# Optimization experiments

Measured on AMD Instinct MI355X. Metric: run time of the kernel, lower is better.

## Reference

```python
import jax, jax.numpy as jnp
import numpy as np

BN_EPS = 1e-5


def conv2d(x, w, b, stride, pad):
    # x: [N,C,H,W], w: [O,I,kh,kw]
    y = jax.lax.conv_general_dilated(
        x, w, window_strides=(stride, stride),
        padding=[(pad, pad), (pad, pad)],
        dimension_numbers=('NCHW', 'OIHW', 'NCHW'))
    return y + b[None, :, None, None]


def batchnorm(x, gamma, beta):
    # training-mode BN: batch stats over (N,H,W) per channel
    m = x.mean(axis=(0, 2, 3), keepdims=True)
    v = x.var(axis=(0, 2, 3), keepdims=True)
    xn = (x - m) * jax.lax.rsqrt(v + BN_EPS)
    return gamma[None, :, None, None] * xn + beta[None, :, None, None]


def setup_inputs() -> dict:
    key = jax.random.key(0)
    ks = jax.random.split(key, 8)
    H = W = 1024
    x = jax.random.normal(ks[0], (1, 3, H, W), dtype=jnp.float32)
    # conv1: 3 -> 32, k3
    w1 = jax.random.normal(ks[1], (32, 3, 3, 3), dtype=jnp.float32) * 0.1
    b1 = jnp.zeros((32,), jnp.float32)
    # conv2: 1 -> 16, k3 s2 p2
    w2 = jax.random.normal(ks[2], (16, 1, 3, 3), dtype=jnp.float32) * 0.1
    b2 = jnp.zeros((16,), jnp.float32)
    g2 = jnp.ones((16,), jnp.float32)
    bt2 = jnp.zeros((16,), jnp.float32)
    # conv3: 16 -> 32, k3 s2 p2
    w3 = jax.random.normal(ks[3], (32, 16, 3, 3), dtype=jnp.float32) * 0.1
    b3 = jnp.zeros((32,), jnp.float32)
    g3 = jnp.ones((32,), jnp.float32)
    bt3 = jnp.zeros((32,), jnp.float32)
    return {'x': x, 'w1': w1, 'b1': b1, 'w2': w2, 'b2': b2, 'g2': g2,
            'bt2': bt2, 'w3': w3, 'b3': b3, 'g3': g3, 'bt3': bt3}


def reference(x, w1, b1, w2, b2, g2, bt2, w3, b3, g3, bt3):
    out = conv2d(x, w1, b1, stride=1, pad=2)          # [1,32,H+2,W+2]
    f = out[0]                                         # [32,H',W'] (Gram uses batch 0 only)
    gram = jnp.einsum('chw,dhw->cd', f, f)             # [32,32] single GEMM instead of O(n^2) loop
    gram = gram[None, None, :, :]                      # [1,1,32,32]
    h = jax.nn.relu(batchnorm(conv2d(gram, w2, b2, stride=2, pad=2), g2, bt2))  # [1,16,17,17]
    h = jax.nn.relu(batchnorm(conv2d(h, w3, b3, stride=2, pad=2), g3, bt3))     # [1,32,10,10]
    return h.mean(axis=(2, 3), keepdims=True)          # AdaptiveAvgPool2d((1,1)) -> [1,32,1,1]
```

## Files before the change

kernel.cpp:

```cpp
#include <hip/hip_runtime.h>

#define NTILES_X 65
#define NTILES   (65*65)
#define OHW      1026
#define NCHUNK   32
#define NBLK     1024
#define NXCD     8
#define BAND     529

typedef unsigned int  uint;
typedef unsigned short ushort;
typedef float  floatx16 __attribute__((ext_vector_type(16)));
typedef __bf16 bf16x8   __attribute__((ext_vector_type(8)));

__device__ __forceinline__ uint pk2f(float a, float b) {
    ushort lo = __builtin_bit_cast(ushort, (__bf16)a);
    ushort hi = __builtin_bit_cast(ushort, (__bf16)b);
    return (uint)lo | ((uint)hi << 16);
}
__device__ __forceinline__ bf16x8 frag_of(uint a, uint b, uint c, uint d) {
    uint4 u = make_uint4(a, b, c, d);
    return __builtin_bit_cast(bf16x8, u);
}
__device__ __forceinline__ constexpr int koff_of(int k) {
    return (k / 9) * 324 + ((k % 9) / 3) * 18 + (k % 3);
}
__device__ __forceinline__ uint bslot(const ushort* buf, int base, int h, int ka, int kb) {
    if (kb < 27) {
        int off = h ? koff_of(kb) : koff_of(ka);
        return (uint)buf[base + off];
    } else if (ka < 27) {
        uint cst = (kb == 27) ? 0x3F80u : 0u;
        uint rd  = (uint)buf[base + koff_of(ka)];
        return h ? cst : rd;
    } else {
        uint ca  = (ka == 27) ? 0x3F80u : 0u;
        uint cb2 = (kb == 27) ? 0x3F80u : 0u;
        return h ? cb2 : ca;
    }
}

__global__ __launch_bounds__(256, 4) void k_conv_gram(
    const float* __restrict__ x,
    const float* __restrict__ w1,
    const float* __restrict__ b1,
    float* __restrict__ partial,
    int nblk)
{
    __shared__ __align__(16) ushort sInB[2][976];
    __shared__ __align__(16) float  gep[4096];

    const int t    = threadIdx.x;
    const int wv   = t >> 6;
    const int lane = t & 63;
    const int h    = lane >> 5;
    const int c    = lane & 31;

    const float b1c = b1[c];
    uint wu0[4], wu1[4];
#pragma unroll
    for (int q = 0; q < 4; ++q) {
        {
            int k0 = h * 8 + 2 * q;
            wu0[q] = pk2f(w1[c * 27 + k0], w1[c * 27 + k0 + 1]);
        }
        {
            int k0 = 16 + h * 8 + 2 * q, k1 = k0 + 1;
            float r0 = w1[c * 27 + (k0 < 27 ? k0 : 26)];
            float r1 = w1[c * 27 + (k1 < 27 ? k1 : 26)];
            float v0 = (k0 < 27) ? r0 : (k0 == 27 ? b1c : 0.f);
            float v1 = (k1 < 27) ? r1 : (k1 == 27 ? b1c : 0.f);
            wu1[q] = pk2f(v0, v1);
        }
    }

    floatx16 gacc;
#pragma unroll
    for (int i = 0; i < 16; ++i) gacc[i] = 0.f;

    const int xcd    = blockIdx.x & (NXCD - 1);
    const int lb     = blockIdx.x >> 3;
    const int nb_per = nblk >> 3;
    const int tstart = xcd * BAND;
    const int tend   = (tstart + BAND < NTILES) ? tstart + BAND : NTILES;

    auto loadregs = [&](int tile, float* v) {
        const int ty = tile / NTILES_X;
        const int tx = tile - ty * NTILES_X;
        const int by = ty * 16, bx = tx * 16;
        const bool interior = (ty >= 1) & (ty <= 62) & (tx >= 1) & (tx <= 62);
#pragma unroll
        for (int j = 0; j < 4; ++j) {
            const int i = t + 256 * j;
            if (j == 3 && i >= 972) { v[j] = 0.f; continue; }
            int ic = i / 324, rem = i - ic * 324, r = rem / 18, cc = rem - r * 18;
            if (interior) {
                v[j] = x[ic * 1048576 + (by - 2 + r) * 1024 + (bx - 2 + cc)];
            } else {
                int iy = by - 2 + r, ix = bx - 2 + cc;
                v[j] = ((unsigned)iy < 1024u && (unsigned)ix < 1024u)
                         ? x[ic * 1048576 + iy * 1024 + ix] : 0.f;
            }
        }
    };
    auto writebuf = [&](int buf, const float* v) {
#pragma unroll
        for (int j = 0; j < 4; ++j) {
            const int i = t + 256 * j;
            if (j == 3 && i >= 972) continue;
            sInB[buf][i] = __builtin_bit_cast(ushort, (__bf16)v[j]);
        }
    };

    int tile = tstart + lb;
    int cur  = 0;
    {
        float v[4];
        loadregs(tile, v);
        writebuf(0, v);
    }
    __syncthreads();

    for (; tile < tend; ) {
        const int nxt = tile + nb_per;
        const bool hasNext = nxt < tend;
        float vn[4];
        if (hasNext) loadregs(nxt, vn);

        {
            const int ty = tile / NTILES_X;
            const int tx = tile - ty * NTILES_X;
            const int by = ty * 16, bx = tx * 16;
            const bool needmask = (ty == 64) | (tx == 64);
            const ushort* bufp = &sInB[cur][0];

#pragma unroll
            for (int e = 0; e < 2; ++e) {
                const int cb   = 2 * wv + e;
                const int base = (cb * 2 + (c >> 4)) * 18 + (c & 15);

                floatx16 cacc;
#pragma unroll
                for (int i = 0; i < 16; ++i) cacc[i] = 0.f;

                uint bu[4];
#pragma unroll
                for (int q = 0; q < 4; ++q) {
                    uint lo = bslot(bufp, base, h, 2*q,     2*q + 8);
                    uint hi = bslot(bufp, base, h, 2*q + 1, 2*q + 9);
                    bu[q] = lo | (hi << 16);
                }
                cacc = __builtin_amdgcn_mfma_f32_32x32x16_bf16(
                    frag_of(bu[0], bu[1], bu[2], bu[3]),
                    frag_of(wu0[0], wu0[1], wu0[2], wu0[3]), cacc, 0, 0, 0);
#pragma unroll
                for (int q = 0; q < 4; ++q) {
                    uint lo = bslot(bufp, base, h, 16 + 2*q,     16 + 2*q + 8);
                    uint hi = bslot(bufp, base, h, 16 + 2*q + 1, 16 + 2*q + 9);
                    bu[q] = lo | (hi << 16);
                }
                cacc = __builtin_amdgcn_mfma_f32_32x32x16_bf16(
                    frag_of(bu[0], bu[1], bu[2], bu[3]),
                    frag_of(wu1[0], wu1[1], wu1[2], wu1[3]), cacc, 0, 0, 0);

                uint pa[4], pb[4];
#pragma unroll
                for (int q2 = 0; q2 < 4; ++q2) {
                    pa[q2] = pk2f(cacc[2*q2],     cacc[2*q2 + 1]);
                    pb[q2] = pk2f(cacc[8 + 2*q2], cacc[8 + 2*q2 + 1]);
                }
                if (needmask) {
                    const uint rA = (uint)((by + 2*cb)     < OHW);
                    const uint rB = (uint)((by + 2*cb + 1) < OHW);
#pragma unroll
                    for (int q2 = 0; q2 < 4; ++q2) {
                        const int q  = q2 >> 1, mm = 2 * (q2 & 1);
                        const uint x0 = (uint)((bx + 8*q + 4*h + mm)     < OHW);
                        const uint x1 = (uint)((bx + 8*q + 4*h + mm + 1) < OHW);
                        pa[q2] &= ((rA & x0) ? 0x0000FFFFu : 0u) | ((rA & x1) ? 0xFFFF0000u : 0u);
                        pb[q2] &= ((rB & x0) ? 0x0000FFFFu : 0u) | ((rB & x1) ? 0xFFFF0000u : 0u);
                    }
                }
                bf16x8 fa = frag_of(pa[0], pa[1], pa[2], pa[3]);
                bf16x8 fb = frag_of(pb[0], pb[1], pb[2], pb[3]);
                gacc = __builtin_amdgcn_mfma_f32_32x32x16_bf16(fa, fa, gacc, 0, 0, 0);
                gacc = __builtin_amdgcn_mfma_f32_32x32x16_bf16(fb, fb, gacc, 0, 0, 0);
            }
        }

        if (hasNext) writebuf(cur ^ 1, vn);
        __syncthreads();
        cur ^= 1;
        tile = nxt;
    }

#pragma unroll
    for (int r = 0; r < 16; ++r) {
        const int row = (r & 3) + 8 * (r >> 2) + 4 * h;
        gep[wv * 1024 + row * 32 + c] = gacc[r];
    }
    __syncthreads();
    {
        const int e = t * 4;
        float s[4] = {0.f, 0.f, 0.f, 0.f};
#pragma unroll
        for (int w = 0; w < 4; ++w) {
            float v[4];
            *(float4*)v = *(const float4*)&gep[w * 1024 + e];
#pragma unroll
            for (int j = 0; j < 4; ++j) s[j] += v[j];
        }
        *(float4*)&partial[(size_t)blockIdx.x * 1024 + e] = *(float4*)s;
    }
}

__global__ __launch_bounds__(256) void k_reduce(
    const float* __restrict__ partial, float* __restrict__ partial2, int nblk)
{
    const int gt    = blockIdx.x * 256 + threadIdx.x;
    const int e     = gt & 1023;
    const int chunk = gt >> 10;
    float s = 0.f;
    for (int b = chunk; b < nblk; b += NCHUNK) s += partial[(size_t)b * 1024 + e];
    partial2[chunk * 1024 + e] = s;
}

__global__ __launch_bounds__(1024) void k_mid(
    const float* __restrict__ partial2,
    const float* __restrict__ w2, const float* __restrict__ b2,
    const float* __restrict__ g2, const float* __restrict__ bt2,
    float* __restrict__ y1pG)
{
    __shared__ float G_pad[36 * 36];
    __shared__ float y1[16 * 289];
    __shared__ float m1[16], r1[16];
    __shared__ float sw2[144], sp2[48];

    const int t = threadIdx.x;

    float s0 = 0.f, s1 = 0.f, s2 = 0.f, s3 = 0.f;
#pragma unroll
    for (int k = 0; k < NCHUNK; k += 4) {
        s0 += partial2[(k + 0) * 1024 + t];
        s1 += partial2[(k + 1) * 1024 + t];
        s2 += partial2[(k + 2) * 1024 + t];
        s3 += partial2[(k + 3) * 1024 + t];
    }
    const float g = (s0 + s1) + (s2 + s3);

    for (int i = t; i < 1296; i += 1024) G_pad[i] = 0.f;
    for (int i = t; i < 144; i += 1024) sw2[i] = w2[i];
    if (t < 16)              sp2[t] = b2[t];
    else if (t < 32)         sp2[t] = g2[t - 16];
    else if (t < 48)         sp2[t] = bt2[t - 32];
    __syncthreads();

    G_pad[((t >> 5) + 2) * 36 + (t & 31) + 2] = g;
    __syncthreads();

    for (int idx = t; idx < 16 * 289; idx += 1024) {
        const int oc = idx / 289;
        const int r  = idx - oc * 289;
        const int oy = r / 17, ox = r - (r / 17) * 17;
        const float* gp = &G_pad[(2 * oy) * 36 + 2 * ox];
        const float* wr = &sw2[oc * 9];
        float s = sp2[oc];
#pragma unroll
        for (int ky = 0; ky < 3; ++ky)
#pragma unroll
            for (int kx = 0; kx < 3; ++kx)
                s = fmaf(gp[ky * 36 + kx], wr[ky * 3 + kx], s);
        y1[idx] = s;
    }
    __syncthreads();

    {
        const int ch = t >> 6, j = t & 63;
        float s = 0.f, ss = 0.f;
        for (int i = j; i < 289; i += 64) {
            float v = y1[ch * 289 + i];
            s += v; ss += v * v;
        }
#pragma unroll
        for (int o = 32; o; o >>= 1) { s += __shfl_xor(s, o); ss += __shfl_xor(ss, o); }
        if (j == 0) {
            float m = s * (1.f / 289.f);
            float var = ss * (1.f / 289.f) - m * m;
            m1[ch] = m;
            r1[ch] = rsqrtf(var + 1e-5f);
        }
    }
    __syncthreads();

    for (int idx = t; idx < 16 * 441; idx += 1024) {
        const int ic  = idx / 441;
        const int rem = idx - ic * 441;
        const int yy  = rem / 21, xx = rem - yy * 21;
        float v = 0.f;
        if (yy >= 2 && yy < 19 && xx >= 2 && xx < 19) {
            float raw = y1[ic * 289 + (yy - 2) * 17 + (xx - 2)];
            v = (raw - m1[ic]) * r1[ic] * sp2[16 + ic] + sp2[32 + ic];
            v = v > 0.f ? v : 0.f;
        }
        y1pG[idx] = v;
    }
}

__global__ __launch_bounds__(256) void k_c3(
    const float* __restrict__ y1pG,
    const float* __restrict__ w3, const float* __restrict__ b3,
    const float* __restrict__ g3, const float* __restrict__ bt3,
    float* __restrict__ out)
{
    __shared__ float yL[16 * 441];
    __shared__ float y2L[128];

    const int t  = threadIdx.x;
    const int oc = blockIdx.x;

    for (int i = t; i < 7056; i += 256) yL[i] = y1pG[i];
    if (t >= 100 && t < 128) y2L[t] = 0.f;
    __syncthreads();

    if (t < 100) {
        const int oy = t / 10, ox = t - 10 * (t / 10);
        const float* wr = w3 + oc * 144;
        float a0 = b3[oc], a1 = 0.f, a2 = 0.f;
#pragma unroll
        for (int ic = 0; ic < 16; ++ic) {
            const float* yi = &yL[ic * 441 + (2 * oy) * 21 + 2 * ox];
            const float* wi = wr + ic * 9;
#pragma unroll
            for (int kx = 0; kx < 3; ++kx) {
                a0 = fmaf(yi[kx],      wi[kx],     a0);
                a1 = fmaf(yi[21 + kx], wi[3 + kx], a1);
                a2 = fmaf(yi[42 + kx], wi[6 + kx], a2);
            }
        }
        y2L[t] = (a0 + a1) + a2;
    }
    __syncthreads();

    if (t < 64) {
        const float x0 = y2L[t], x1 = y2L[t + 64];
        float s = x0 + x1, ss = x0 * x0 + x1 * x1;
#pragma unroll
        for (int o = 32; o; o >>= 1) { s += __shfl_xor(s, o); ss += __shfl_xor(ss, o); }
        const float m  = s * 0.01f;
        const float var = ss * 0.01f - m * m;
        const float rs = rsqrtf(var + 1e-5f);
        const float gg = g3[oc], bb = bt3[oc];
        float a = 0.f;
        if (t < 100) { float f = (x0 - m) * rs * gg + bb; a += f > 0.f ? f : 0.f; }
        if (t < 36)  { float f = (x1 - m) * rs * gg + bb; a += f > 0.f ? f : 0.f; }
#pragma unroll
        for (int o = 32; o; o >>= 1) a += __shfl_xor(a, o);
        if (t == 0) out[oc] = a * 0.01f;
    }
}

extern "C" void kernel_launch(void* const* d_in, const int* in_sizes, int n_in,
                              void* d_out, int out_size, void* d_ws, size_t ws_size,
                              hipStream_t stream)
{
    const float* x   = (const float*)d_in[0];
    const float* w1  = (const float*)d_in[1];
    const float* b1  = (const float*)d_in[2];
    const float* w2  = (const float*)d_in[3];
    const float* b2  = (const float*)d_in[4];
    const float* g2  = (const float*)d_in[5];
    const float* bt2 = (const float*)d_in[6];
    const float* w3  = (const float*)d_in[7];
    const float* b3  = (const float*)d_in[8];
    const float* g3  = (const float*)d_in[9];
    const float* bt3 = (const float*)d_in[10];

    int nblk = NBLK;

    float* P    = (float*)d_ws;
    float* P2   = P + (size_t)nblk * 1024;
    float* y1pG = P2 + (size_t)NCHUNK * 1024;
    float* out  = (float*)d_out;

    k_conv_gram<<<nblk, 256, 0, stream>>>(x, w1, b1, P, nblk);
    k_reduce<<<128, 256, 0, stream>>>(P, P2, nblk);
    k_mid<<<1, 1024, 0, stream>>>(P2, w2, b2, g2, bt2, y1pG);
    k_c3<<<32, 256, 0, stream>>>(y1pG, w3, b3, g3, bt3, out);
}
```

Before: 41.58 us.

## Fuse mid-stage and conv3 tail into one kernel with redundant per-block compute

Merges the single-block conv2/BN stage and the 32-block conv3/BN/pool kernel into one launch. Each of the 32 blocks now recomputes the Gram reduction, conv2 and BN2 redundantly in shared memory, so the global round-trip of the padded intermediate and one kernel launch go away. Conv3 is also split across two thread groups over input channels and then summed. The cost is 32x redundant small compute and larger shared memory per block.

Result: faster. 39.39 us (-5.3%).

```diff
diff --git a/kernel.cpp b/kernel.cpp
--- a/kernel.cpp
+++ b/kernel.cpp
@@ -225,46 +225,55 @@
     partial2[chunk * 1024 + e] = s;
 }
 
-__global__ __launch_bounds__(1024) void k_mid(
+__global__ __launch_bounds__(256) void k_tail2(
     const float* __restrict__ partial2,
     const float* __restrict__ w2, const float* __restrict__ b2,
     const float* __restrict__ g2, const float* __restrict__ bt2,
-    float* __restrict__ y1pG)
+    const float* __restrict__ w3, const float* __restrict__ b3,
+    const float* __restrict__ g3, const float* __restrict__ bt3,
+    float* __restrict__ out)
 {
     __shared__ float G_pad[36 * 36];
     __shared__ float y1[16 * 289];
+    __shared__ float y1p[16 * 21 * 21];
+    __shared__ float y2L[256];
     __shared__ float m1[16], r1[16];
     __shared__ float sw2[144], sp2[48];
 
-    const int t = threadIdx.x;
-
-    float s0 = 0.f, s1 = 0.f, s2 = 0.f, s3 = 0.f;
-#pragma unroll
-    for (int k = 0; k < NCHUNK; k += 4) {
-        s0 += partial2[(k + 0) * 1024 + t];
-        s1 += partial2[(k + 1) * 1024 + t];
-        s2 += partial2[(k + 2) * 1024 + t];
-        s3 += partial2[(k + 3) * 1024 + t];
-    }
-    const float g = (s0 + s1) + (s2 + s3);
-
-    for (int i = t; i < 1296; i += 1024) G_pad[i] = 0.f;
-    for (int i = t; i < 144; i += 1024) sw2[i] = w2[i];
-    if (t < 16)              sp2[t] = b2[t];
-    else if (t < 32)         sp2[t] = g2[t - 16];
-    else if (t < 48)         sp2[t] = bt2[t - 32];
-    __syncthreads();
-
-    G_pad[((t >> 5) + 2) * 36 + (t & 31) + 2] = g;
-    __syncthreads();
-
-    for (int idx = t; idx < 16 * 289; idx += 1024) {
-        const int oc = idx / 289;
-        const int r  = idx - oc * 289;
+    const int t  = threadIdx.x;
+    const int oc = blockIdx.x;
+
+    float gv[4] = {0.f, 0.f, 0.f, 0.f};
+#pragma unroll
+    for (int k = 0; k < NCHUNK; ++k) {
+        float v[4];
+        *(float4*)v = *(const float4*)&partial2[k * 1024 + t * 4];
+#pragma unroll
+        for (int j = 0; j < 4; ++j) gv[j] += v[j];
+    }
+
+    for (int i = t; i < 1296; i += 256) G_pad[i] = 0.f;
+    for (int i = t; i < 7056; i += 256) y1p[i] = 0.f;
+    if (t < 144) sw2[t] = w2[t];
+    if (t >= 160 && t < 176)      sp2[t - 160]      = b2[t - 160];
+    else if (t >= 176 && t < 192) sp2[t - 160]      = g2[t - 176];
+    else if (t >= 192 && t < 208) sp2[t - 160]      = bt2[t - 192];
+    __syncthreads();
+
+#pragma unroll
+    for (int j = 0; j < 4; ++j) {
+        const int e = t * 4 + j;
+        G_pad[((e >> 5) + 2) * 36 + (e & 31) + 2] = gv[j];
+    }
+    __syncthreads();
+
+    for (int idx = t; idx < 16 * 289; idx += 256) {
+        const int c2 = idx / 289;
+        const int r  = idx - c2 * 289;
         const int oy = r / 17, ox = r - (r / 17) * 17;
         const float* gp = &G_pad[(2 * oy) * 36 + 2 * ox];
-        const float* wr = &sw2[oc * 9];
-        float s = sp2[oc];
+        const float* wr = &sw2[c2 * 9];
+        float s = sp2[c2];
 #pragma unroll
         for (int ky = 0; ky < 3; ++ky)
 #pragma unroll
@@ -275,14 +284,16 @@
     __syncthreads();
 
     {
-        const int ch = t >> 6, j = t & 63;
+        const int lane = t & 63;
+        const int ch   = (t >> 6) * 4 + (lane >> 4);
+        const int j    = lane & 15;
         float s = 0.f, ss = 0.f;
-        for (int i = j; i < 289; i += 64) {
+        for (int i = j; i < 289; i += 16) {
             float v = y1[ch * 289 + i];
             s += v; ss += v * v;
         }
 #pragma unroll
-        for (int o = 32; o; o >>= 1) { s += __shfl_xor(s, o); ss += __shfl_xor(ss, o); }
+        for (int o = 8; o; o >>= 1) { s += __shfl_xor(s, o); ss += __shfl_xor(ss, o); }
         if (j == 0) {
             float m = s * (1.f / 289.f);
             float var = ss * (1.f / 289.f) - m * m;
@@ -292,53 +303,41 @@
     }
     __syncthreads();
 
-    for (int idx = t; idx < 16 * 441; idx += 1024) {
-        const int ic  = idx / 441;
-        const int rem = idx - ic * 441;
-        const int yy  = rem / 21, xx = rem - yy * 21;
-        float v = 0.f;
-        if (yy >= 2 && yy < 19 && xx >= 2 && xx < 19) {
-            float raw = y1[ic * 289 + (yy - 2) * 17 + (xx - 2)];
-            v = (raw - m1[ic]) * r1[ic] * sp2[16 + ic] + sp2[32 + ic];
-            v = v > 0.f ? v : 0.f;
-        }
-        y1pG[idx] = v;
-    }
-}
-
-__global__ __launch_bounds__(256) void k_c3(
-    const float* __restrict__ y1pG,
-    const float* __restrict__ w3, const float* __restrict__ b3,
-    const float* __restrict__ g3, const float* __restrict__ bt3,
-    float* __restrict__ out)
-{
-    __shared__ float yL[16 * 441];
-    __shared__ float y2L[128];
-
-    const int t  = threadIdx.x;
-    const int oc = blockIdx.x;
-
-    for (int i = t; i < 7056; i += 256) yL[i] = y1pG[i];
+    for (int idx = t; idx < 16 * 289; idx += 256) {
+        const int c2 = idx / 289;
+        const int r  = idx - c2 * 289;
+        const int oy = r / 17, ox = r - (r / 17) * 17;
+        float v = (y1[idx] - m1[c2]) * r1[c2] * sp2[16 + c2] + sp2[32 + c2];
+        y1p[c2 * 441 + (oy + 2) * 21 + ox + 2] = v > 0.f ? v : 0.f;
+    }
     if (t >= 100 && t < 128) y2L[t] = 0.f;
     __syncthreads();
 
-    if (t < 100) {
-        const int oy = t / 10, ox = t - 10 * (t / 10);
-        const float* wr = w3 + oc * 144;
-        float a0 = b3[oc], a1 = 0.f, a2 = 0.f;
-#pragma unroll
-        for (int ic = 0; ic < 16; ++ic) {
-            const float* yi = &yL[ic * 441 + (2 * oy) * 21 + 2 * ox];
-            const float* wi = wr + ic * 9;
-#pragma unroll
-            for (int kx = 0; kx < 3; ++kx) {
-                a0 = fmaf(yi[kx],      wi[kx],     a0);
-                a1 = fmaf(yi[21 + kx], wi[3 + kx], a1);
-                a2 = fmaf(yi[42 + kx], wi[6 + kx], a2);
+    {
+        const int grp = t >> 7;
+        const int px  = t & 127;
+        if (px < 100) {
+            const int oy = px / 10, ox = px - 10 * (px / 10);
+            const float* wr = w3 + oc * 144 + grp * 72;
+            float a0 = 0.f, a1 = 0.f, a2 = 0.f;
+#pragma unroll
+            for (int ic8 = 0; ic8 < 8; ++ic8) {
+                const int ic = grp * 8 + ic8;
+                const float* yi = &y1p[ic * 441 + (2 * oy) * 21 + 2 * ox];
+                const float* wi = wr + ic8 * 9;
+#pragma unroll
+                for (int kx = 0; kx < 3; ++kx) {
+                    a0 = fmaf(yi[kx],      wi[kx],     a0);
+                    a1 = fmaf(yi[21 + kx], wi[3 + kx], a1);
+                    a2 = fmaf(yi[42 + kx], wi[6 + kx], a2);
+                }
             }
-        }
-        y2L[t] = (a0 + a1) + a2;
-    }
+            y2L[grp * 128 + px] = (a0 + a1) + a2;
+        }
+    }
+    __syncthreads();
+
+    if (t < 100) y2L[t] = y2L[t] + y2L[128 + t] + b3[oc];
     __syncthreads();
 
     if (t < 64) {
@@ -346,10 +345,10 @@
         float s = x0 + x1, ss = x0 * x0 + x1 * x1;
 #pragma unroll
         for (int o = 32; o; o >>= 1) { s += __shfl_xor(s, o); ss += __shfl_xor(ss, o); }
-        const float m  = s * 0.01f;
+        const float m   = s * 0.01f;
         const float var = ss * 0.01f - m * m;
-        const float rs = rsqrtf(var + 1e-5f);
-        const float gg = g3[oc], bb = bt3[oc];
+        const float rs  = rsqrtf(var + 1e-5f);
+        const float gg  = g3[oc], bb = bt3[oc];
         float a = 0.f;
         if (t < 100) { float f = (x0 - m) * rs * gg + bb; a += f > 0.f ? f : 0.f; }
         if (t < 36)  { float f = (x1 - m) * rs * gg + bb; a += f > 0.f ? f : 0.f; }
@@ -377,13 +376,11 @@
 
     int nblk = NBLK;
 
-    float* P    = (float*)d_ws;
-    float* P2   = P + (size_t)nblk * 1024;
-    float* y1pG = P2 + (size_t)NCHUNK * 1024;
-    float* out  = (float*)d_out;
+    float* P   = (float*)d_ws;
+    float* P2  = P + (size_t)nblk * 1024;
+    float* out = (float*)d_out;
 
     k_conv_gram<<<nblk, 256, 0, stream>>>(x, w1, b1, P, nblk);
     k_reduce<<<128, 256, 0, stream>>>(P, P2, nblk);
-    k_mid<<<1, 1024, 0, stream>>>(P2, w2, b2, g2, bt2, y1pG);
-    k_c3<<<32, 256, 0, stream>>>(y1pG, w3, b3, g3, bt3, out);
-}
+    k_tail2<<<32, 256, 0, stream>>>(P2, w2, b2, g2, bt2, w3, b3, g3, bt3, out);
+}
```
